# Kernel optimization log

Hardware: AMD Instinct MI355X
Metric: run time of the kernel (lower is better)

## Reference

```python
import jax, jax.numpy as jnp
import numpy as np
import math

D = 128      # d_model == num_filters
L = 4        # num_conv_layers
K = 7        # kernel_size
H = 8        # num_heads
B, S = 64, 400


def setup_inputs() -> dict:
    key = jax.random.key(0)
    ks = jax.random.split(key, 24)
    s = 0.02
    inp = {}
    inp['x'] = jax.random.normal(ks[0], (B, S, D), dtype=jnp.float32)
    # per-conv-layer params (stacked over L)
    inp['ln_g'] = jnp.ones((L, D), jnp.float32)
    inp['ln_b'] = jnp.zeros((L, D), jnp.float32)
    inp['dw_w'] = jax.random.normal(ks[1], (L, D, D, K), dtype=jnp.float32) * s
    inp['dw_b'] = jnp.zeros((L, D), jnp.float32)
    inp['pw_w'] = jax.random.normal(ks[2], (L, D, D), dtype=jnp.float32) * s
    inp['pw_b'] = jnp.zeros((L, D), jnp.float32)
    # attention block
    inp['attln_g'] = jnp.ones((D,), jnp.float32)
    inp['attln_b'] = jnp.zeros((D,), jnp.float32)
    inp['wq'] = jax.random.normal(ks[3], (D, D), dtype=jnp.float32) * s
    inp['bq'] = jnp.zeros((D,), jnp.float32)
    inp['wk'] = jax.random.normal(ks[4], (D, D), dtype=jnp.float32) * s
    inp['bk'] = jnp.zeros((D,), jnp.float32)
    inp['wv'] = jax.random.normal(ks[5], (D, D), dtype=jnp.float32) * s
    inp['bv'] = jnp.zeros((D,), jnp.float32)
    inp['wp'] = jax.random.normal(ks[6], (D, D), dtype=jnp.float32) * s
    inp['bp'] = jnp.zeros((D,), jnp.float32)
    # ffn
    inp['ffnln_g'] = jnp.ones((D,), jnp.float32)
    inp['ffnln_b'] = jnp.zeros((D,), jnp.float32)
    inp['fc_w'] = jax.random.normal(ks[7], (D, D), dtype=jnp.float32) * s
    inp['fc_b'] = jnp.zeros((D,), jnp.float32)
    return inp


def _layernorm(x, g, b, eps=1e-5):
    mu = jnp.mean(x, axis=-1, keepdims=True)
    var = jnp.var(x, axis=-1, keepdims=True)
    return (x - mu) * jax.lax.rsqrt(var + eps) * g + b


def _pos_encoding(seq_len, channels, dtype):
    pos = jnp.arange(seq_len, dtype=dtype)                       # [S]
    freq = 1.0 / (10000.0 ** (jnp.arange(0, channels, 2, dtype=dtype) / channels))
    sin_inp = pos[:, None] * freq[None, :]                       # [S, C/2]
    return jnp.concatenate([jnp.sin(sin_inp), jnp.cos(sin_inp)], axis=-1)  # [S, C]


def _encoder_fwd(x, ln_g, ln_b, dw_w, dw_b, pw_w, pw_b,
                 attln_g, attln_b, wq, bq, wk, bk, wv, bv, wp, bp,
                 ffnln_g, ffnln_b, fc_w, fc_b):
    b, s, d = x.shape
    out = x + _pos_encoding(s, d, x.dtype)[None, :, :]

    # conv stack: LN -> transpose -> (full) conv K -> pointwise conv -> transpose
    pad = dw_w.shape[-1] // 2
    for i in range(dw_w.shape[0]):
        h = _layernorm(out, ln_g[i], ln_b[i])
        t = jnp.transpose(h, (0, 2, 1))                          # [B, D, S]
        t = jax.lax.conv_general_dilated(
            t, dw_w[i], window_strides=(1,), padding=[(pad, pad)],
            dimension_numbers=('NCH', 'OIH', 'NCH')) + dw_b[i][None, :, None]
        t = jnp.einsum('bds,fd->bfs', t, pw_w[i]) + pw_b[i][None, :, None]
        out = jnp.transpose(t, (0, 2, 1))                        # [B, S, D]

    # causal self-attention (explicit scores, per original)
    h = _layernorm(out, attln_g, attln_b)
    hd = d // H
    q = (jnp.einsum('bsd,od->bso', h, wq) + bq).reshape(b, s, H, hd)
    k = (jnp.einsum('bsd,od->bso', h, wk) + bk).reshape(b, s, H, hd)
    v = (jnp.einsum('bsd,od->bso', h, wv) + bv).reshape(b, s, H, hd)
    att = jnp.einsum('bqhd,bkhd->bhqk', q, k) / math.sqrt(hd)    # [B, H, S, S]
    causal = jnp.tril(jnp.ones((s, s), dtype=bool))
    att = jnp.where(causal[None, None], att, jnp.asarray(-1e10, att.dtype))
    att = jax.nn.softmax(att, axis=-1)
    y = jnp.einsum('bhqk,bkhd->bqhd', att, v).reshape(b, s, d)
    y = jnp.einsum('bsd,od->bso', y, wp) + bp

    # ffn
    y = _layernorm(y, ffnln_g, ffnln_b)
    y = jnp.einsum('bsd,od->bso', y, fc_w) + fc_b
    return jax.nn.relu(y)


def reference(x, ln_g, ln_b, dw_w, dw_b, pw_w, pw_b,
              attln_g, attln_b, wq, bq, wk, bk, wv, bv, wp, bp,
              ffnln_g, ffnln_b, fc_w, fc_b):
    return _encoder_fwd(x, ln_g, ln_b, dw_w, dw_b, pw_w, pw_b,
                        attln_g, attln_b, wq, bq, wk, bk, wv, bv, wp, bp,
                        ffnln_g, ffnln_b, fc_w, fc_b)
```

## Files before the change

kernel.cpp:

```cpp
#include <hip/hip_runtime.h>
#include <hip/hip_bf16.h>
#include <math.h>

#define Dm 128
#define Lc 4
#define Kc 7
#define Hh 8
#define Bb 64
#define Ss 400
#define SsP 448
#define TOK (Bb*Ss)

typedef __attribute__((ext_vector_type(8))) short bf16x8;
typedef __attribute__((ext_vector_type(4))) float f32x4;

__device__ __forceinline__ float bf2f(unsigned int u) {
    union { unsigned int i; float f; } x; x.i = u << 16; return x.f;
}
__device__ __forceinline__ unsigned short f2bf(float f) {
    __hip_bfloat16 h = __float2bfloat16(f);
    return __builtin_bit_cast(unsigned short, h);
}
__device__ __forceinline__ unsigned int packbf(float a, float b) {
    return (unsigned int)f2bf(a) | ((unsigned int)f2bf(b) << 16);
}


__global__ __launch_bounds__(256) void prep_all(const float* __restrict__ wq, const float* __restrict__ wk,
                                                const float* __restrict__ wv, const float* __restrict__ wp,
                                                const float* __restrict__ fc,
                                                const float* __restrict__ pw_w, const float* __restrict__ dw_w,
                                                const float* __restrict__ dw_b, const float* __restrict__ pw_b,
                                                float* __restrict__ pe, unsigned short* __restrict__ wf,
                                                float* __restrict__ mb, unsigned short* __restrict__ mwf) {
    __shared__ unsigned short hiS[64][136];
    __shared__ unsigned short loS[64][136];
    int blk = blockIdx.x;
    int tid = threadIdx.x;
    if (blk < 200) {
        int s = blk * 2 + (tid >> 7);
        int c = tid & 127;
        int j = (c < 64) ? c : (c - 64);
        float freq = expf(-(2.0f * j / 128.0f) * 9.210340371976184f);
        float a = (float)s * freq;
        pe[s * Dm + c] = (c < 64) ? sinf(a) : cosf(a);
        return;
    }
    if (blk < 520) {
        int idx = (blk - 200) * 256 + tid;
        int m = idx >> 14;
        int r = idx & 16383;
        int fragi = r >> 9, lr = (r >> 3) & 63, j = r & 7;
        int kb = fragi >> 3, nb = fragi & 7;
        int o = nb * 16 + (lr & 15);
        int d = kb * 32 + (lr >> 4) * 8 + j;
        const float* src = (m == 0) ? wq : (m == 1) ? wk : (m == 2) ? wv : (m == 3) ? wp : fc;
        wf[idx] = f2bf(src[o * Dm + d]);
        return;
    }
    if (blk < 524) {
        int l = blk - 520;
        int f = tid;
        if (f < Dm) {
            const float* pwl = pw_w + ((size_t)l * Dm + f) * Dm;
            const float* db  = dw_b + l * Dm;
            float acc = pw_b[l * Dm + f];
            #pragma unroll 8
            for (int c4 = 0; c4 < 32; ++c4) {
                float4 p = *(const float4*)(pwl + c4 * 4);
                float4 d = *(const float4*)(db + c4 * 4);
                acc += p.x * d.x + p.y * d.y + p.z * d.z + p.w * d.w;
            }
            mb[l * Dm + f] = acc;
        }
        return;
    }
    int mblk = blk - 524;
    int ih = mblk & 1;
    int k  = (mblk >> 1) % 7;
    int l  = mblk / 14;
    int lane = tid & 63, w = tid >> 6;

    const float* dwl = dw_w + (size_t)l * (Dm * Dm * Kc) + k;
    for (int it = 0; it < 32; ++it) {
        int idx = it * 256 + tid;
        int c = idx >> 6, il = idx & 63;
        int i = ih * 64 + il;
        float x = dwl[(size_t)(c * Dm + i) * Kc];
        unsigned short hi = f2bf(x);
        float lo = x - bf2f(hi);
        hiS[il][c] = hi;
        loS[il][c] = f2bf(lo);
    }
    __syncthreads();

    const float* pwl = pw_w + (size_t)l * Dm * Dm;
    int arow = lane & 15, ac = (lane >> 4) * 8;
    f32x4 acc[2][4];
    #pragma unroll
    for (int n = 0; n < 2; ++n)
        #pragma unroll
        for (int m = 0; m < 4; ++m) acc[n][m] = (f32x4){0.f, 0.f, 0.f, 0.f};

    #pragma unroll
    for (int kb = 0; kb < 4; ++kb) {
        int c0 = kb * 32 + ac;
        bf16x8 Bhi[2], Blo[2];
        #pragma unroll
        for (int n = 0; n < 2; ++n) {
            int f = (w * 2 + n) * 16 + arow;
            const float* rp = pwl + (size_t)f * Dm + c0;
            float4 a = *(const float4*)rp;
            float4 b = *(const float4*)(rp + 4);
            float v[8] = {a.x, a.y, a.z, a.w, b.x, b.y, b.z, b.w};
            unsigned short hh[8], ll[8];
            #pragma unroll
            for (int j = 0; j < 8; ++j) {
                hh[j] = f2bf(v[j]);
                ll[j] = f2bf(v[j] - bf2f(hh[j]));
            }
            uint4 uh = make_uint4((unsigned)hh[0] | ((unsigned)hh[1] << 16),
                                  (unsigned)hh[2] | ((unsigned)hh[3] << 16),
                                  (unsigned)hh[4] | ((unsigned)hh[5] << 16),
                                  (unsigned)hh[6] | ((unsigned)hh[7] << 16));
            uint4 ul = make_uint4((unsigned)ll[0] | ((unsigned)ll[1] << 16),
                                  (unsigned)ll[2] | ((unsigned)ll[3] << 16),
                                  (unsigned)ll[4] | ((unsigned)ll[5] << 16),
                                  (unsigned)ll[6] | ((unsigned)ll[7] << 16));
            Bhi[n] = __builtin_bit_cast(bf16x8, uh);
            Blo[n] = __builtin_bit_cast(bf16x8, ul);
        }
        #pragma unroll
        for (int m = 0; m < 4; ++m) {
            bf16x8 ahi = *(const bf16x8*)&hiS[m * 16 + arow][c0];
            bf16x8 alo = *(const bf16x8*)&loS[m * 16 + arow][c0];
            #pragma unroll
            for (int n = 0; n < 2; ++n) {
                acc[n][m] = __builtin_amdgcn_mfma_f32_16x16x32_bf16(ahi, Bhi[n], acc[n][m], 0, 0, 0);
                acc[n][m] = __builtin_amdgcn_mfma_f32_16x16x32_bf16(ahi, Blo[n], acc[n][m], 0, 0, 0);
                acc[n][m] = __builtin_amdgcn_mfma_f32_16x16x32_bf16(alo, Bhi[n], acc[n][m], 0, 0, 0);
            }
        }
    }
    #pragma unroll
    for (int n = 0; n < 2; ++n) {
        int nb = w * 2 + n;
        #pragma unroll
        for (int m = 0; m < 4; ++m) {
            int i0 = ih * 64 + m * 16 + (lane >> 4) * 4;
            int ib = i0 >> 5, i32 = i0 & 31;
            int lanep = ((i32 >> 3) << 4) | arow;
            int jb = i32 & 7;
            size_t frag = ((size_t)(l * 28 + (k * 4 + ib)) * 8 + nb);
            *(uint2*)(mwf + frag * 512 + lanep * 8 + jb) =
                make_uint2(packbf(acc[n][m][0], acc[n][m][1]),
                           packbf(acc[n][m][2], acc[n][m][3]));
        }
    }
}


__device__ __forceinline__ uint4 ln_core(float v[8],
                                         const float* __restrict__ g,
                                         const float* __restrict__ b, int c16) {
    float sum = 0.f, sq = 0.f;
    #pragma unroll
    for (int j = 0; j < 8; ++j) { sum += v[j]; sq += v[j] * v[j]; }
    #pragma unroll
    for (int off = 8; off; off >>= 1) {
        sum += __shfl_xor(sum, off);
        sq  += __shfl_xor(sq, off);
    }
    float mu = sum * (1.0f / 128.0f);
    float var = sq * (1.0f / 128.0f) - mu * mu;
    float rs = rsqrtf(var + 1e-5f);
    float4 g0 = *(const float4*)(g + c16 * 8);
    float4 g1 = *(const float4*)(g + c16 * 8 + 4);
    float4 b0 = *(const float4*)(b + c16 * 8);
    float4 b1 = *(const float4*)(b + c16 * 8 + 4);
    uint4 o;
    o.x = packbf((v[0] - mu) * rs * g0.x + b0.x, (v[1] - mu) * rs * g0.y + b0.y);
    o.y = packbf((v[2] - mu) * rs * g0.z + b0.z, (v[3] - mu) * rs * g0.w + b0.w);
    o.z = packbf((v[4] - mu) * rs * g1.x + b1.x, (v[5] - mu) * rs * g1.y + b1.y);
    o.w = packbf((v[6] - mu) * rs * g1.z + b1.z, (v[7] - mu) * rs * g1.w + b1.w);
    return o;
}

__device__ __forceinline__ uint4 ln_pack_bf(const unsigned short* __restrict__ rp,
                                            const float* __restrict__ g,
                                            const float* __restrict__ b, int c16) {
    uint4 u = *(const uint4*)rp;
    float v[8] = { bf2f(u.x & 0xffffu), bf2f(u.x >> 16), bf2f(u.y & 0xffffu), bf2f(u.y >> 16),
                   bf2f(u.z & 0xffffu), bf2f(u.z >> 16), bf2f(u.w & 0xffffu), bf2f(u.w >> 16) };
    return ln_core(v, g, b, c16);
}


__global__ __launch_bounds__(512) void mega(const float* __restrict__ x,
                                            const float* __restrict__ pe,
                                            const unsigned short* __restrict__ mwf,
                                            const float* __restrict__ mb,
                                            const float* __restrict__ ln_g,
                                            const float* __restrict__ ln_b,
                                            const float* __restrict__ attg,
                                            const float* __restrict__ attb,
                                            const unsigned short* __restrict__ wfb,
                                            const float* __restrict__ bq,
                                            const float* __restrict__ bk,
                                            const float* __restrict__ bv,
                                            unsigned short* __restrict__ Qo,
                                            unsigned short* __restrict__ Ko,
                                            unsigned short* __restrict__ Vo) {
    __shared__ unsigned short L[118][136];
    __shared__ unsigned short R[101][128];
    int tid = threadIdx.x, lane = tid & 63, w = tid >> 6;
    int bI = blockIdx.x / 5;
    int s0 = (blockIdx.x % 5) * 80;
    int arow = lane & 15, acol = (lane >> 4) * 8, rr = (lane >> 4) * 4;
    int nb0 = (w & 3) * 2, mh = w >> 2;

    for (int c = tid; c < 118 * 16; c += 512) {
        int idx = c >> 4, c16 = c & 15;
        int g = s0 - 12 + idx;
        uint4 o = make_uint4(0u, 0u, 0u, 0u);
        if (g >= 0 && g < Ss) {
            const float* rp = x + ((size_t)bI * Ss + g) * Dm + c16 * 8;
            const float* pp = pe + (size_t)g * Dm + c16 * 8;
            float v[8];
            #pragma unroll
            for (int j = 0; j < 8; ++j) v[j] = rp[j] + pp[j];
            o = ln_core(v, ln_g, ln_b, c16);
        }
        *(uint4*)&L[idx][c16 * 8] = o;
    }
    __syncthreads();

    const int NT[4] = {7, 6, 6, 5};
    for (int l = 0; l < 4; ++l) {
        int in_lo = 3 * l;
        int out_lo = 3 * (l + 1), out_hi = 104 - 3 * (l + 1);
        int ntiles = NT[l];
        const unsigned short* mw = mwf + (size_t)l * 114688;

        f32x4 acc[2][4];
        #pragma unroll
        for (int n = 0; n < 2; ++n)
            #pragma unroll
            for (int mi = 0; mi < 4; ++mi) acc[n][mi] = (f32x4){0.f, 0.f, 0.f, 0.f};

        #pragma unroll 4
        for (int kb = 0; kb < 28; ++kb) {
            int k = kb >> 2, i0 = (kb & 3) * 32;
            bf16x8 b0 = *(const bf16x8*)(mw + ((size_t)(kb * 8 + nb0)) * 512 + lane * 8);
            bf16x8 b1 = *(const bf16x8*)(mw + ((size_t)(kb * 8 + nb0 + 1)) * 512 + lane * 8);
            #pragma unroll
            for (int mi = 0; mi < 4; ++mi) {
                int m = mh + 2 * mi;
                if (m < ntiles) {
                    bf16x8 af = *(const bf16x8*)&L[in_lo + m * 16 + arow + k][i0 + acol];
                    acc[0][mi] = __builtin_amdgcn_mfma_f32_16x16x32_bf16(af, b0, acc[0][mi], 0, 0, 0);
                    acc[1][mi] = __builtin_amdgcn_mfma_f32_16x16x32_bf16(af, b1, acc[1][mi], 0, 0, 0);
                }
            }
        }
        __syncthreads();
        #pragma unroll
        for (int n = 0; n < 2; ++n) {
            int f = (nb0 + n) * 16 + arow;
            float bias = mb[l * Dm + f];
            #pragma unroll
            for (int mi = 0; mi < 4; ++mi) {
                int m = mh + 2 * mi;
                if (m < ntiles) {
                    #pragma unroll
                    for (int r = 0; r < 4; ++r) {
                        int o = out_lo + m * 16 + rr + r;
                        if (o < out_hi) R[o][f] = f2bf(acc[n][mi][r] + bias);
                    }
                }
            }
        }
        __syncthreads();

        if (l < 3) {
            const float* lg = ln_g + (l + 1) * Dm;
            const float* lb = ln_b + (l + 1) * Dm;
            int span = out_hi - out_lo;
            for (int c = tid; c < span * 16; c += 512) {
                int idx = out_lo + (c >> 4), c16 = c & 15;
                int g = s0 - 12 + idx;
                uint4 o = make_uint4(0u, 0u, 0u, 0u);
                if (g >= 0 && g < Ss)
                    o = ln_pack_bf(&R[idx][c16 * 8], lg, lb, c16);
                *(uint4*)&L[idx][c16 * 8] = o;
            }
        } else {
            for (int c = tid; c < 80 * 16; c += 512) {
                int idx = 12 + (c >> 4), c16 = c & 15;
                *(uint4*)&L[idx][c16 * 8] = ln_pack_bf(&R[idx][c16 * 8], attg, attb, c16);
            }
        }
        __syncthreads();
    }

    for (int mat = 0; mat < 3; ++mat) {
        const unsigned short* wf = wfb + (size_t)mat * 16384;
        f32x4 acc[2][3];
        #pragma unroll
        for (int n = 0; n < 2; ++n)
            #pragma unroll
            for (int mi = 0; mi < 3; ++mi) acc[n][mi] = (f32x4){0.f, 0.f, 0.f, 0.f};
        #pragma unroll
        for (int kb = 0; kb < 4; ++kb) {
            bf16x8 b0 = *(const bf16x8*)(wf + ((size_t)(kb * 8 + nb0)) * 512 + lane * 8);
            bf16x8 b1 = *(const bf16x8*)(wf + ((size_t)(kb * 8 + nb0 + 1)) * 512 + lane * 8);
            #pragma unroll
            for (int mi = 0; mi < 3; ++mi) {
                int m = mh + 2 * mi;
                if (m < 5) {
                    bf16x8 af = *(const bf16x8*)&L[12 + m * 16 + arow][kb * 32 + acol];
                    acc[0][mi] = __builtin_amdgcn_mfma_f32_16x16x32_bf16(af, b0, acc[0][mi], 0, 0, 0);
                    acc[1][mi] = __builtin_amdgcn_mfma_f32_16x16x32_bf16(af, b1, acc[1][mi], 0, 0, 0);
                }
            }
        }
        const float* bias = (mat == 0) ? bq : (mat == 1) ? bk : bv;
        float sc = (mat == 0) ? 0.25f : 1.0f;
        #pragma unroll
        for (int n = 0; n < 2; ++n) {
            int hI = nb0 + n;
            float bvv = bias[hI * 16 + arow];
            if (mat < 2) {
                unsigned short* qo = (mat == 0) ? Qo : Ko;
                #pragma unroll
                for (int mi = 0; mi < 3; ++mi) {
                    int m = mh + 2 * mi;
                    if (m < 5) {
                        #pragma unroll
                        for (int r = 0; r < 4; ++r) {
                            int s = s0 + m * 16 + rr + r;
                            qo[(((size_t)(bI * Hh + hI)) * Ss + s) * 16 + arow] =
                                f2bf((acc[n][mi][r] + bvv) * sc);
                        }
                    }
                }
            } else {
                unsigned short* base = Vo + ((size_t)(bI * Hh + hI) * 16 + arow) * SsP + s0;
                #pragma unroll
                for (int mi = 0; mi < 3; ++mi) {
                    int m = mh + 2 * mi;
                    if (m < 5) {
                        unsigned lo = packbf(acc[n][mi][0] + bvv, acc[n][mi][1] + bvv);
                        unsigned hi = packbf(acc[n][mi][2] + bvv, acc[n][mi][3] + bvv);
                        *(uint2*)(base + m * 16 + rr) = make_uint2(lo, hi);
                    }
                }
            }
        }
    }
}


__global__ __launch_bounds__(256) void gemm2(const unsigned short* __restrict__ in,
                                             const unsigned short* __restrict__ wf,
                                             const float* __restrict__ bias,
                                             const float* __restrict__ lng,
                                             const float* __restrict__ lnb,
                                             void* __restrict__ outv, int mode) {
    __shared__ unsigned short hs[80][136];
    int tid = threadIdx.x;
    int lane = tid & 63, w = tid >> 6;
    size_t tok0 = (size_t)blockIdx.x * 80;
    const unsigned short* ib = in + tok0 * Dm;
    if (lng) {
        for (int c = tid; c < 80 * 16; c += 256) {
            int row = c >> 4, c16 = c & 15;
            *(uint4*)&hs[row][c16 * 8] = ln_pack_bf(ib + (size_t)row * Dm + c16 * 8, lng, lnb, c16);
        }
    } else {
        for (int c = tid; c < 80 * 16; c += 256) {
            int row = c >> 4, c16 = c & 15;
            *(uint4*)&hs[row][c16 * 8] = *(const uint4*)(ib + (size_t)row * Dm + c16 * 8);
        }
    }
    __syncthreads();

    f32x4 acc[2][5];
    #pragma unroll
    for (int n = 0; n < 2; ++n)
        #pragma unroll
        for (int m = 0; m < 5; ++m) acc[n][m] = (f32x4){0.f, 0.f, 0.f, 0.f};

    int nb0 = w * 2;
    int arow = lane & 15, acol = (lane >> 4) * 8;
    #pragma unroll
    for (int kb = 0; kb < 4; ++kb) {
        bf16x8 b0 = *(const bf16x8*)(wf + ((size_t)(kb * 8 + nb0)) * 512 + lane * 8);
        bf16x8 b1 = *(const bf16x8*)(wf + ((size_t)(kb * 8 + nb0 + 1)) * 512 + lane * 8);
        #pragma unroll
        for (int m = 0; m < 5; ++m) {
            bf16x8 af = *(const bf16x8*)&hs[m * 16 + arow][kb * 32 + acol];
            acc[0][m] = __builtin_amdgcn_mfma_f32_16x16x32_bf16(af, b0, acc[0][m], 0, 0, 0);
            acc[1][m] = __builtin_amdgcn_mfma_f32_16x16x32_bf16(af, b1, acc[1][m], 0, 0, 0);
        }
    }
    int rr = (lane >> 4) * 4;
    #pragma unroll
    for (int n = 0; n < 2; ++n) {
        int f0 = (nb0 + n) * 16;
        float bvv = bias[f0 + arow];
        #pragma unroll
        for (int m = 0; m < 5; ++m)
            #pragma unroll
            for (int r = 0; r < 4; ++r) {
                float v = acc[n][m][r] + bvv;
                if (mode == 1) {
                    ((float*)outv)[(tok0 + m * 16 + rr + r) * Dm + f0 + arow] = fmaxf(v, 0.f);
                } else {
                    ((unsigned short*)outv)[(tok0 + m * 16 + rr + r) * Dm + f0 + arow] = f2bf(v);
                }
            }
    }
}


__global__ __launch_bounds__(320) void attn_mfma(const unsigned short* __restrict__ Q,
                                                 const unsigned short* __restrict__ Kb,
                                                 const unsigned short* __restrict__ VT,
                                                 unsigned short* __restrict__ out) {
    int wid = threadIdx.x >> 6, lane = threadIdx.x & 63;
    int bh = blockIdx.x;
    int qt = blockIdx.y * 5 + wid;
    int q15 = lane & 15, h = lane >> 4;
    int qg = qt * 16 + q15;

    uint4 qv = make_uint4(0u, 0u, 0u, 0u);
    if (h < 2) qv = *(const uint4*)(Q + ((size_t)bh * Ss + qg) * 16 + h * 8);
    bf16x8 qf = __builtin_bit_cast(bf16x8, qv);

    f32x4 o = (f32x4){0.f, 0.f, 0.f, 0.f};
    float mrow = -1e30f, lrow = 0.f;
    const unsigned short* kbase = Kb + (size_t)bh * Ss * 16;
    const unsigned short* vbase = VT + ((size_t)bh * 16 + q15) * SsP;
    int srcA = q15 + ((h & 1) << 5);
    int srcB = srcA + 16;
    bool t1 = h >= 2;
    f32x4 z = (f32x4){0.f, 0.f, 0.f, 0.f};

    for (int kt0 = 0; kt0 <= qt; kt0 += 4) {
        uint4 kv[4];
        #pragma unroll
        for (int t = 0; t < 4; ++t) {
            kv[t] = make_uint4(0u, 0u, 0u, 0u);
            if (h < 2 && kt0 + t <= qt)
                kv[t] = *(const uint4*)(kbase + (size_t)((kt0 + t) * 16 + q15) * 16 + h * 8);
        }
        f32x4 s[4];
        #pragma unroll
        for (int t = 0; t < 4; ++t)
            s[t] = __builtin_amdgcn_mfma_f32_16x16x32_bf16(__builtin_bit_cast(bf16x8, kv[t]), qf, z, 0, 0, 0);

        float p[16];
        #pragma unroll
        for (int t = 0; t < 4; ++t)
            #pragma unroll
            for (int r = 0; r < 4; ++r) {
                int ka = (kt0 + t) * 16 + h * 4 + r;
                p[t * 4 + r] = (ka <= qg) ? s[t][r] : -1e30f;
            }
        float tm = p[0];
        #pragma unroll
        for (int i = 1; i < 16; ++i) tm = fmaxf(tm, p[i]);
        tm = fmaxf(tm, __shfl_xor(tm, 16));
        tm = fmaxf(tm, __shfl_xor(tm, 32));
        float mnew = fmaxf(mrow, tm);
        float corr = __expf(mrow - mnew);
        float psum = 0.f;
        #pragma unroll
        for (int i = 0; i < 16; ++i) { p[i] = __expf(p[i] - mnew); psum += p[i]; }
        psum += __shfl_xor(psum, 16);
        psum += __shfl_xor(psum, 32);
        lrow = lrow * corr + psum;
        mrow = mnew;
        o[0] *= corr; o[1] *= corr; o[2] *= corr; o[3] *= corr;

        #pragma unroll
        for (int pr = 0; pr < 2; ++pr) {
            const float* pp = p + pr * 8;
            unsigned pk0 = packbf(pp[0], pp[1]), pk1 = packbf(pp[2], pp[3]);
            unsigned pk2 = packbf(pp[4], pp[5]), pk3 = packbf(pp[6], pp[7]);
            unsigned a0 = __shfl(pk0, srcA), a1 = __shfl(pk1, srcA);
            unsigned a2 = __shfl(pk0, srcB), a3 = __shfl(pk1, srcB);
            unsigned b0 = __shfl(pk2, srcA), b1 = __shfl(pk3, srcA);
            unsigned b2 = __shfl(pk2, srcB), b3 = __shfl(pk3, srcB);
            uint4 pw = make_uint4(t1 ? b0 : a0, t1 ? b1 : a1, t1 ? b2 : a2, t1 ? b3 : a3);
            uint4 vv = *(const uint4*)(vbase + (kt0 + pr * 2) * 16 + h * 8);
            o = __builtin_amdgcn_mfma_f32_16x16x32_bf16(__builtin_bit_cast(bf16x8, vv),
                                                        __builtin_bit_cast(bf16x8, pw), o, 0, 0, 0);
        }
    }
    float inv = 1.0f / lrow;
    int bI = bh >> 3, hh = bh & 7;
    unsigned short* op = out + ((size_t)bI * Ss + qg) * Dm + hh * 16 + h * 4;
    *(uint2*)op = make_uint2(packbf(o[0] * inv, o[1] * inv),
                             packbf(o[2] * inv, o[3] * inv));
}


extern "C" void kernel_launch(void* const* d_in, const int* in_sizes, int n_in,
                              void* d_out, int out_size, void* d_ws, size_t ws_size,
                              hipStream_t stream) {
    (void)in_sizes; (void)n_in; (void)out_size; (void)ws_size;
    const float* x       = (const float*)d_in[0];
    const float* ln_g    = (const float*)d_in[1];
    const float* ln_b    = (const float*)d_in[2];
    const float* dw_w    = (const float*)d_in[3];
    const float* dw_b    = (const float*)d_in[4];
    const float* pw_w    = (const float*)d_in[5];
    const float* pw_b    = (const float*)d_in[6];
    const float* attln_g = (const float*)d_in[7];
    const float* attln_b = (const float*)d_in[8];
    const float* wq = (const float*)d_in[9];
    const float* bq = (const float*)d_in[10];
    const float* wk = (const float*)d_in[11];
    const float* bk = (const float*)d_in[12];
    const float* wv = (const float*)d_in[13];
    const float* bv = (const float*)d_in[14];
    const float* wp = (const float*)d_in[15];
    const float* bp = (const float*)d_in[16];
    const float* ffnln_g = (const float*)d_in[17];
    const float* ffnln_b = (const float*)d_in[18];
    const float* fc_w = (const float*)d_in[19];
    const float* fc_b = (const float*)d_in[20];

    float* ws = (float*)d_ws;
    float* pe = ws;
    float* mb = pe + 51200;
    unsigned short* mwf = (unsigned short*)(mb + 512);
    unsigned short* wfb = mwf + 458752;
    unsigned short* Qb  = wfb + 81920;
    unsigned short* Kb2 = Qb + 3276800;
    unsigned short* VTb = Kb2 + 3276800;
    unsigned short* A1b = VTb + 3670016;
    unsigned short* C1  = A1b + 3276800;

    prep_all<<<580, 256, 0, stream>>>(wq, wk, wv, wp, fc_w, pw_w, dw_w, dw_b, pw_b,
                                      pe, wfb, mb, mwf);

    mega<<<320, 512, 0, stream>>>(x, pe, mwf, mb, ln_g, ln_b, attln_g, attln_b,
                                  wfb, bq, bk, bv, Qb, Kb2, VTb);

    attn_mfma<<<dim3(512, 5), 320, 0, stream>>>(Qb, Kb2, VTb, A1b);
    gemm2<<<320, 256, 0, stream>>>(A1b, wfb + 3 * 16384, bp, nullptr, nullptr, C1, 0);

    gemm2<<<320, 256, 0, stream>>>(C1, wfb + 4 * 16384, fc_b, ffnln_g, ffnln_b, d_out, 1);
}
```

Baseline: 121.3 us.

## Enlarge conv-stack token tile to 100, swizzle LDS, separate R buffer

The fused conv+QKV kernel now handles 100 tokens per block instead of 80, so it launches 256 blocks rather than 320. This cuts the relative overhead of the 12-row halo that each block recomputes through the four conv layers. The padded LDS arrays are replaced by XOR-swizzled unpadded layouts to avoid bank conflicts. R is offset so it no longer aliases L, which lets the barrier before the R writes be removed. In exchange each block does more work, some rows are clamped or masked, and 256 blocks may leave compute units unevenly loaded.

```diff
diff --git a/kernel.cpp b/kernel.cpp
--- a/kernel.cpp
+++ b/kernel.cpp
@@ -186,15 +186,23 @@
     return o;
 }
 
+__device__ __forceinline__ uint4 ln_unpack_core(uint4 u,
+                                                const float* __restrict__ g,
+                                                const float* __restrict__ b, int c16) {
+    float v[8] = { bf2f(u.x & 0xffffu), bf2f(u.x >> 16), bf2f(u.y & 0xffffu), bf2f(u.y >> 16),
+                   bf2f(u.z & 0xffffu), bf2f(u.z >> 16), bf2f(u.w & 0xffffu), bf2f(u.w >> 16) };
+    return ln_core(v, g, b, c16);
+}
+
 __device__ __forceinline__ uint4 ln_pack_bf(const unsigned short* __restrict__ rp,
                                             const float* __restrict__ g,
                                             const float* __restrict__ b, int c16) {
-    uint4 u = *(const uint4*)rp;
-    float v[8] = { bf2f(u.x & 0xffffu), bf2f(u.x >> 16), bf2f(u.y & 0xffffu), bf2f(u.y >> 16),
-                   bf2f(u.z & 0xffffu), bf2f(u.z >> 16), bf2f(u.w & 0xffffu), bf2f(u.w >> 16) };
-    return ln_core(v, g, b, c16);
-}
-
+    return ln_unpack_core(*(const uint4*)rp, g, b, c16);
+}
+
+
+#define LROWS 124
+#define RROWS 118
 
 __global__ __launch_bounds__(512) void mega(const float* __restrict__ x,
                                             const float* __restrict__ pe,
@@ -211,15 +219,15 @@
                                             unsigned short* __restrict__ Qo,
                                             unsigned short* __restrict__ Ko,
                                             unsigned short* __restrict__ Vo) {
-    __shared__ unsigned short L[118][136];
-    __shared__ unsigned short R[101][128];
+    __shared__ unsigned short Lf[LROWS * 128];
+    __shared__ unsigned short Rf[RROWS * 128];
     int tid = threadIdx.x, lane = tid & 63, w = tid >> 6;
-    int bI = blockIdx.x / 5;
-    int s0 = (blockIdx.x % 5) * 80;
-    int arow = lane & 15, acol = (lane >> 4) * 8, rr = (lane >> 4) * 4;
+    int bI = blockIdx.x >> 2;
+    int s0 = (blockIdx.x & 3) * 100;
+    int arow = lane & 15, h = lane >> 4, rr = h * 4;
     int nb0 = (w & 3) * 2, mh = w >> 2;
 
-    for (int c = tid; c < 118 * 16; c += 512) {
+    for (int c = tid; c < LROWS * 16; c += 512) {
         int idx = c >> 4, c16 = c & 15;
         int g = s0 - 12 + idx;
         uint4 o = make_uint4(0u, 0u, 0u, 0u);
@@ -231,14 +239,14 @@
             for (int j = 0; j < 8; ++j) v[j] = rp[j] + pp[j];
             o = ln_core(v, ln_g, ln_b, c16);
         }
-        *(uint4*)&L[idx][c16 * 8] = o;
+        *(uint4*)(Lf + idx * 128 + ((c16 ^ (idx & 7)) << 3)) = o;
     }
     __syncthreads();
 
-    const int NT[4] = {7, 6, 6, 5};
+    const int NT[4] = {8, 7, 7, 7};
     for (int l = 0; l < 4; ++l) {
         int in_lo = 3 * l;
-        int out_lo = 3 * (l + 1), out_hi = 104 - 3 * (l + 1);
+        int out_lo = 3 * (l + 1), out_hi = LROWS - 3 * (l + 1);
         int ntiles = NT[l];
         const unsigned short* mw = mwf + (size_t)l * 114688;
 
@@ -250,23 +258,25 @@
 
         #pragma unroll 4
         for (int kb = 0; kb < 28; ++kb) {
-            int k = kb >> 2, i0 = (kb & 3) * 32;
+            int k = kb >> 2, blk0 = (kb & 3) * 4 + h;
             bf16x8 b0 = *(const bf16x8*)(mw + ((size_t)(kb * 8 + nb0)) * 512 + lane * 8);
             bf16x8 b1 = *(const bf16x8*)(mw + ((size_t)(kb * 8 + nb0 + 1)) * 512 + lane * 8);
             #pragma unroll
             for (int mi = 0; mi < 4; ++mi) {
                 int m = mh + 2 * mi;
                 if (m < ntiles) {
-                    bf16x8 af = *(const bf16x8*)&L[in_lo + m * 16 + arow + k][i0 + acol];
+                    int ar = in_lo + m * 16 + arow + k;
+                    if (ar > LROWS - 1) ar = LROWS - 1;
+                    bf16x8 af = *(const bf16x8*)(Lf + ar * 128 + ((blk0 ^ (ar & 7)) << 3));
                     acc[0][mi] = __builtin_amdgcn_mfma_f32_16x16x32_bf16(af, b0, acc[0][mi], 0, 0, 0);
                     acc[1][mi] = __builtin_amdgcn_mfma_f32_16x16x32_bf16(af, b1, acc[1][mi], 0, 0, 0);
                 }
             }
         }
-        __syncthreads();
         #pragma unroll
         for (int n = 0; n < 2; ++n) {
             int f = (nb0 + n) * 16 + arow;
+            int fblk = f >> 3, flo = f & 7;
             float bias = mb[l * Dm + f];
             #pragma unroll
             for (int mi = 0; mi < 4; ++mi) {
@@ -275,7 +285,10 @@
                     #pragma unroll
                     for (int r = 0; r < 4; ++r) {
                         int o = out_lo + m * 16 + rr + r;
-                        if (o < out_hi) R[o][f] = f2bf(acc[n][mi][r] + bias);
+                        if (o < out_hi) {
+                            int rw = o - 3;
+                            Rf[rw * 128 + ((fblk ^ (rw & 7)) << 3) + flo] = f2bf(acc[n][mi][r] + bias);
+                        }
                     }
                 }
             }
@@ -290,14 +303,19 @@
                 int idx = out_lo + (c >> 4), c16 = c & 15;
                 int g = s0 - 12 + idx;
                 uint4 o = make_uint4(0u, 0u, 0u, 0u);
-                if (g >= 0 && g < Ss)
-                    o = ln_pack_bf(&R[idx][c16 * 8], lg, lb, c16);
-                *(uint4*)&L[idx][c16 * 8] = o;
+                if (g >= 0 && g < Ss) {
+                    int rw = idx - 3;
+                    uint4 u = *(const uint4*)(Rf + rw * 128 + ((c16 ^ (rw & 7)) << 3));
+                    o = ln_unpack_core(u, lg, lb, c16);
+                }
+                *(uint4*)(Lf + idx * 128 + ((c16 ^ (idx & 7)) << 3)) = o;
             }
         } else {
-            for (int c = tid; c < 80 * 16; c += 512) {
+            for (int c = tid; c < 100 * 16; c += 512) {
                 int idx = 12 + (c >> 4), c16 = c & 15;
-                *(uint4*)&L[idx][c16 * 8] = ln_pack_bf(&R[idx][c16 * 8], attg, attb, c16);
+                int rw = idx - 3;
+                uint4 u = *(const uint4*)(Rf + rw * 128 + ((c16 ^ (rw & 7)) << 3));
+                *(uint4*)(Lf + idx * 128 + ((c16 ^ (idx & 7)) << 3)) = ln_unpack_core(u, attg, attb, c16);
             }
         }
         __syncthreads();
@@ -305,20 +323,22 @@
 
     for (int mat = 0; mat < 3; ++mat) {
         const unsigned short* wf = wfb + (size_t)mat * 16384;
-        f32x4 acc[2][3];
+        f32x4 acc[2][4];
         #pragma unroll
         for (int n = 0; n < 2; ++n)
             #pragma unroll
-            for (int mi = 0; mi < 3; ++mi) acc[n][mi] = (f32x4){0.f, 0.f, 0.f, 0.f};
+            for (int mi = 0; mi < 4; ++mi) acc[n][mi] = (f32x4){0.f, 0.f, 0.f, 0.f};
         #pragma unroll
         for (int kb = 0; kb < 4; ++kb) {
+            int blk0 = kb * 4 + h;
             bf16x8 b0 = *(const bf16x8*)(wf + ((size_t)(kb * 8 + nb0)) * 512 + lane * 8);
             bf16x8 b1 = *(const bf16x8*)(wf + ((size_t)(kb * 8 + nb0 + 1)) * 512 + lane * 8);
             #pragma unroll
-            for (int mi = 0; mi < 3; ++mi) {
+            for (int mi = 0; mi < 4; ++mi) {
                 int m = mh + 2 * mi;
-                if (m < 5) {
-                    bf16x8 af = *(const bf16x8*)&L[12 + m * 16 + arow][kb * 32 + acol];
+                if (m < 7) {
+                    int ar = 12 + m * 16 + arow;
+                    bf16x8 af = *(const bf16x8*)(Lf + ar * 128 + ((blk0 ^ (ar & 7)) << 3));
                     acc[0][mi] = __builtin_amdgcn_mfma_f32_16x16x32_bf16(af, b0, acc[0][mi], 0, 0, 0);
                     acc[1][mi] = __builtin_amdgcn_mfma_f32_16x16x32_bf16(af, b1, acc[1][mi], 0, 0, 0);
                 }
@@ -333,26 +353,30 @@
             if (mat < 2) {
                 unsigned short* qo = (mat == 0) ? Qo : Ko;
                 #pragma unroll
-                for (int mi = 0; mi < 3; ++mi) {
+                for (int mi = 0; mi < 4; ++mi) {
                     int m = mh + 2 * mi;
-                    if (m < 5) {
+                    if (m < 7) {
                         #pragma unroll
                         for (int r = 0; r < 4; ++r) {
-                            int s = s0 + m * 16 + rr + r;
-                            qo[(((size_t)(bI * Hh + hI)) * Ss + s) * 16 + arow] =
-                                f2bf((acc[n][mi][r] + bvv) * sc);
+                            int lcl = m * 16 + rr + r;
+                            if (lcl < 100) {
+                                int s = s0 + lcl;
+                                qo[(((size_t)(bI * Hh + hI)) * Ss + s) * 16 + arow] =
+                                    f2bf((acc[n][mi][r] + bvv) * sc);
+                            }
                         }
                     }
                 }
             } else {
                 unsigned short* base = Vo + ((size_t)(bI * Hh + hI) * 16 + arow) * SsP + s0;
                 #pragma unroll
-                for (int mi = 0; mi < 3; ++mi) {
+                for (int mi = 0; mi < 4; ++mi) {
                     int m = mh + 2 * mi;
-                    if (m < 5) {
+                    int lcl = m * 16 + rr;
+                    if (m < 7 && lcl < 100) {
                         unsigned lo = packbf(acc[n][mi][0] + bvv, acc[n][mi][1] + bvv);
                         unsigned hi = packbf(acc[n][mi][2] + bvv, acc[n][mi][3] + bvv);
-                        *(uint2*)(base + m * 16 + rr) = make_uint2(lo, hi);
+                        *(uint2*)(base + lcl) = make_uint2(lo, hi);
                     }
                 }
             }
@@ -547,7 +571,7 @@
     prep_all<<<580, 256, 0, stream>>>(wq, wk, wv, wp, fc_w, pw_w, dw_w, dw_b, pw_b,
                                       pe, wfb, mb, mwf);
 
-    mega<<<320, 512, 0, stream>>>(x, pe, mwf, mb, ln_g, ln_b, attln_g, attln_b,
+    mega<<<256, 512, 0, stream>>>(x, pe, mwf, mb, ln_g, ln_b, attln_g, attln_b,
                                   wfb, bq, bk, bv, Qb, Kb2, VTb);
 
     attn_mfma<<<dim3(512, 5), 320, 0, stream>>>(Qb, Kb2, VTb, A1b);
```

Result: slower. 126.8 us (+4.6%).
